# Kernel optimization log

Measured on AMD Instinct MI355X. Metric: run time of the kernel, lower is better.

The kernel has to match this reference:

```python
import jax, jax.numpy as jnp
import numpy as np

HEADS = 16
D_MODEL = 1024
IMG_MODEL = 512
D_K = D_MODEL // HEADS


def setup_inputs() -> dict:
    key = jax.random.key(0)
    ks = jax.random.split(key, 12)
    B, LQ, LKV = 8, 2048, 1024
    s_dm = 1.0 / np.sqrt(D_MODEL)
    s_im = 1.0 / np.sqrt(IMG_MODEL)
    return {
        "q": jax.random.normal(ks[0], (B, LQ, D_MODEL), jnp.float32),
        "k": jax.random.normal(ks[1], (B, LKV, IMG_MODEL), jnp.float32),
        "v": jax.random.normal(ks[2], (B, LKV, IMG_MODEL), jnp.float32),
        "Wq": jax.random.normal(ks[3], (D_MODEL, D_MODEL), jnp.float32) * s_dm,
        "bq": jnp.zeros((D_MODEL,), jnp.float32),
        "Wk": jax.random.normal(ks[4], (IMG_MODEL, D_MODEL), jnp.float32) * s_im,
        "bk": jnp.zeros((D_MODEL,), jnp.float32),
        "Wv": jax.random.normal(ks[5], (IMG_MODEL, D_MODEL), jnp.float32) * s_im,
        "bv": jnp.zeros((D_MODEL,), jnp.float32),
        "Wo": jax.random.normal(ks[6], (D_MODEL, D_MODEL), jnp.float32) * s_dm,
        "bo": jnp.zeros((D_MODEL,), jnp.float32),
    }


def reference(q, k, v, Wq, bq, Wk, bk, Wv, bv, Wo, bo):
    B, LQ, _ = q.shape
    LKV = k.shape[1]
    # projections -> [B, H, L, d_k]
    qh = (q @ Wq + bq).reshape(B, LQ, HEADS, D_K).transpose(0, 2, 1, 3)
    kh = (k @ Wk + bk).reshape(B, LKV, HEADS, D_K).transpose(0, 2, 1, 3)
    vh = (v @ Wv + bv).reshape(B, LKV, HEADS, D_K).transpose(0, 2, 1, 3)
    scale = 1.0 / np.sqrt(D_K)
    scores = jnp.einsum("bhqd,bhkd->bhqk", qh, kh) * scale  # [B,H,LQ,LKV]
    attn = jax.nn.softmax(scores, axis=-1)  # dropout = identity at eval
    out = jnp.einsum("bhqk,bhkd->bhqd", attn, vh)  # [B,H,LQ,d_k]
    concat = out.transpose(0, 2, 1, 3).reshape(B, LQ, D_MODEL)
    return concat @ Wo + bo
```

## Files before the change

### kernel.cpp

```cpp
#include <hip/hip_runtime.h>

typedef __bf16 bf16;
typedef __bf16 bf16x8 __attribute__((ext_vector_type(8)));
typedef __bf16 bf16x4 __attribute__((ext_vector_type(4)));
typedef float f32x4 __attribute__((ext_vector_type(4)));

constexpr int BB   = 8;
constexpr int LQ   = 2048;
constexpr int LKV  = 1024;
constexpr int DM   = 1024;
constexpr int DIMG = 512;
constexpr int H    = 16;
constexpr int DK   = 64;

__device__ inline void async16(const bf16* g, bf16* l) {
  __builtin_amdgcn_global_load_lds((const __attribute__((address_space(1))) void*)g,
                                   (__attribute__((address_space(3))) void*)l, 16, 0, 0);
}
__device__ inline float fexp2(float x) { return __builtin_amdgcn_exp2f(x); }

__global__ __launch_bounds__(256) void cvt_all(const float* __restrict__ q,
                                               const float* __restrict__ k,
                                               const float* __restrict__ v,
                                               bf16* __restrict__ qo,
                                               bf16* __restrict__ ko,
                                               bf16* __restrict__ vo,
                                               int nq4, int nk4) {
  int i = blockIdx.x * 256 + threadIdx.x;
  const float* in;
  bf16* out;
  int idx;
  if (i < nq4) { in = q; out = qo; idx = i; }
  else if (i < nq4 + nk4) { in = k; out = ko; idx = i - nq4; }
  else if (i < nq4 + 2 * nk4) { in = v; out = vo; idx = i - nq4 - nk4; }
  else return;
  const float4 f = ((const float4*)in)[idx];
  bf16x4 o;
  o[0] = (bf16)f.x; o[1] = (bf16)f.y; o[2] = (bf16)f.z; o[3] = (bf16)f.w;
  ((bf16x4*)out)[idx] = o;
}

__global__ __launch_bounds__(256) void transpose_all(const float* __restrict__ Wq,
                                                     const float* __restrict__ Wk,
                                                     const float* __restrict__ Wv,
                                                     const float* __restrict__ Wo,
                                                     bf16* __restrict__ WqT,
                                                     bf16* __restrict__ WkT,
                                                     bf16* __restrict__ WvT,
                                                     bf16* __restrict__ WoT) {
  const int z = blockIdx.z;
  const float* W;
  bf16* WT;
  int K;
  if (z == 0) { W = Wq; WT = WqT; K = DM; }
  else if (z == 1) { W = Wk; WT = WkT; K = DIMG; }
  else if (z == 2) { W = Wv; WT = WvT; K = DIMG; }
  else { W = Wo; WT = WoT; K = DM; }
  const int N = DM;
  if (blockIdx.x * 64 >= K) return;

  __shared__ float tile[64][65];
  const int k0 = blockIdx.x * 64, n0 = blockIdx.y * 64;
  const int tx = threadIdx.x & 63, tg = threadIdx.x >> 6;
#pragma unroll
  for (int i = 0; i < 16; ++i) {
    int row = tg * 16 + i;
    tile[row][tx] = W[(size_t)(k0 + row) * N + n0 + tx];
  }
  __syncthreads();
#pragma unroll
  for (int i = 0; i < 16; ++i) {
    int nrow = tg * 16 + i;
    WT[(size_t)(n0 + nrow) * K + k0 + tx] = (bf16)tile[tx][nrow];
  }
}

template <typename OutT, bool VT_OUT>
__device__ __forceinline__ void gemm_body(const bf16* __restrict__ A,
                                          const bf16* __restrict__ Bt,
                                          const float* __restrict__ bias,
                                          OutT* __restrict__ C,
                                          int N, int K, float oscale, int bm, int bn,
                                          bf16* As, bf16* Bs) {
  const int tid = threadIdx.x, lane = tid & 63, wave = tid >> 6;
  const int wm = (wave & 1) * 64, wn = (wave >> 1) * 64;
  const int fm = lane & 15, quad = lane >> 4, fk8 = quad * 8;

  f32x4 acc[4][4];
#pragma unroll
  for (int i = 0; i < 4; ++i)
#pragma unroll
    for (int j = 0; j < 4; ++j) {
      f32x4 z = {0.f, 0.f, 0.f, 0.f};
      acc[i][j] = z;
    }

  const int srow = lane >> 2, scol = (lane & 3) * 8;
  const bf16* ag0 = A + (size_t)(bm * 128 + wave * 16 + srow) * K + scol;
  const bf16* ag1 = ag0 + (size_t)64 * K;
  const bf16* bg0 = Bt + (size_t)(bn * 128 + wave * 16 + srow) * K + scol;
  const bf16* bg1 = bg0 + (size_t)64 * K;
  bf16* la0 = As + (wave * 16) * 32;
  bf16* la1 = As + (64 + wave * 16) * 32;
  bf16* lb0 = Bs + (wave * 16) * 32;
  bf16* lb1 = Bs + (64 + wave * 16) * 32;

  const int KT = K >> 5;
  async16(ag0, la0);
  async16(ag1, la1);
  async16(bg0, lb0);
  async16(bg1, lb1);
  __syncthreads();

  for (int t = 0; t < KT; ++t) {
    const int cur = (t & 1) * (128 * 32);
    if (t + 1 < KT) {
      const int nxt = ((t + 1) & 1) * (128 * 32);
      const int k0 = (t + 1) * 32;
      async16(ag0 + k0, la0 + nxt);
      async16(ag1 + k0, la1 + nxt);
      async16(bg0 + k0, lb0 + nxt);
      async16(bg1 + k0, lb1 + nxt);
    }
    bf16x8 af[4], bfr[4];
#pragma unroll
    for (int i = 0; i < 4; ++i)
      af[i] = *(const bf16x8*)&As[cur + (wm + i * 16 + fm) * 32 + fk8];
#pragma unroll
    for (int j = 0; j < 4; ++j)
      bfr[j] = *(const bf16x8*)&Bs[cur + (wn + j * 16 + fm) * 32 + fk8];
#pragma unroll
    for (int i = 0; i < 4; ++i)
#pragma unroll
      for (int j = 0; j < 4; ++j)
        acc[i][j] = __builtin_amdgcn_mfma_f32_16x16x32_bf16(af[i], bfr[j], acc[i][j], 0, 0, 0);
    __syncthreads();
  }

#pragma unroll
  for (int j = 0; j < 4; ++j) {
    const int col = bn * 128 + wn + j * 16 + fm;
    const float bv = bias[col];
    if constexpr (VT_OUT) {
      const int h = col >> 6, dk = col & 63;
#pragma unroll
      for (int i = 0; i < 4; ++i) {
        const int row = bm * 128 + wm + i * 16 + quad * 4;
        const int b = row >> 10, t = row & 1023;
        bf16x4 o;
#pragma unroll
        for (int r = 0; r < 4; ++r) o[r] = (bf16)((acc[i][j][r] + bv) * oscale);
        *(bf16x4*)&C[(((size_t)(b * H + h) * DK + dk) << 10) + t] = o;
      }
    } else {
#pragma unroll
      for (int i = 0; i < 4; ++i) {
#pragma unroll
        for (int r = 0; r < 4; ++r) {
          const int row = bm * 128 + wm + i * 16 + quad * 4 + r;
          C[(size_t)row * N + col] = (OutT)((acc[i][j][r] + bv) * oscale);
        }
      }
    }
  }
}

template <typename OutT>
__global__ __launch_bounds__(256) void gemm_one(const bf16* __restrict__ A,
                                                const bf16* __restrict__ Bt,
                                                const float* __restrict__ bias,
                                                OutT* __restrict__ C,
                                                int N, int K, float oscale) {
  __shared__ __align__(16) bf16 As[2 * 128 * 32];
  __shared__ __align__(16) bf16 Bs[2 * 128 * 32];
  const int cpx = gridDim.x >> 3;
  const int wg = ((int)blockIdx.x & 7) * cpx + ((int)blockIdx.x >> 3);
  const int nbn = N >> 7;
  gemm_body<OutT, false>(A, Bt, bias, C, N, K, oscale, wg / nbn, wg % nbn, As, Bs);
}

__global__ __launch_bounds__(256) void gemm_kv(const bf16* __restrict__ kbf,
                                               const bf16* __restrict__ WkT,
                                               const float* __restrict__ bk,
                                               bf16* __restrict__ kh,
                                               const bf16* __restrict__ vbf,
                                               const bf16* __restrict__ WvT,
                                               const float* __restrict__ bv,
                                               bf16* __restrict__ Vt) {
  __shared__ __align__(16) bf16 As[2 * 128 * 32];
  __shared__ __align__(16) bf16 Bs[2 * 128 * 32];
  const int cpx = gridDim.x >> 3;
  const int wg = ((int)blockIdx.x & 7) * cpx + ((int)blockIdx.x >> 3);
  const int bn = wg & 7;
  const int rest = wg >> 3;
  const int bm = rest & 63;
  if (rest < 64)
    gemm_body<bf16, false>(kbf, WkT, bk, kh, DM, DIMG, 1.0f, bm, bn, As, Bs);
  else
    gemm_body<bf16, true>(vbf, WvT, bv, Vt, DM, DIMG, 1.0f, bm, bn, As, Bs);
}

__global__ __launch_bounds__(512, 4) void attn_kernel(const bf16* __restrict__ qh,
                                                      const bf16* __restrict__ kh,
                                                      const bf16* __restrict__ vt,
                                                      bf16* __restrict__ out) {
  constexpr int NT = LKV / 64;
  __shared__ __align__(16) bf16 Ks[2][64 * 64];
  __shared__ __align__(16) bf16 Vs[2][64 * 64];
  __shared__ __align__(16) bf16 Ps[8][32 * 64];

  const int tid = threadIdx.x, lane = tid & 63, w = tid >> 6;
  const int fm = lane & 15, quad = lane >> 4;
  const int qt = blockIdx.x, h = blockIdx.y, b = blockIdx.z;
  const int q0 = qt * 256;

  const bf16* qbase = qh + ((size_t)(b * LQ) + q0 + w * 32) * DM + h * DK;
  const bf16* kbase = kh + (size_t)(b * LKV) * DM + h * DK;
  const bf16* vbase = vt + (size_t)(b * H + h) * DK * LKV;

  bf16x8 qf[2][2];
#pragma unroll
  for (int i = 0; i < 2; ++i)
#pragma unroll
    for (int kg = 0; kg < 2; ++kg)
      qf[i][kg] = *(const bf16x8*)&qbase[(size_t)(i * 16 + fm) * DM + kg * 32 + quad * 8];

  const int srow = lane >> 3, sslot = lane & 7;
  const int fs = fm & 7;

  auto stage = [&](int t, int bf) {
    const int r0 = w * 8;
    const int row = r0 + srow;
    const int gs = (sslot ^ (row & 7)) << 3;
    async16(kbase + (size_t)(t * 64 + row) * DM + gs, &Ks[bf][r0 * 64]);
    async16(vbase + (size_t)row * LKV + t * 64 + gs, &Vs[bf][r0 * 64]);
  };

  stage(0, 0);
  stage(1, 1);

  float row_m[2] = {-1e30f, -1e30f}, row_l[2] = {0.f, 0.f};
  f32x4 o_acc[2][4];
#pragma unroll
  for (int i = 0; i < 2; ++i)
#pragma unroll
    for (int jd = 0; jd < 4; ++jd) {
      f32x4 z = {0.f, 0.f, 0.f, 0.f};
      o_acc[i][jd] = z;
    }

  bf16* Pw = Ps[w];

#pragma unroll 2
  for (int t = 0; t < NT; ++t) {
    asm volatile("s_waitcnt vmcnt(2)" ::: "memory");
    __builtin_amdgcn_s_barrier();
    __builtin_amdgcn_sched_barrier(0);
    const bf16* Kb = Ks[t & 1];
    const bf16* Vb = Vs[t & 1];

    f32x4 s[4][2];
#pragma unroll
    for (int m = 0; m < 4; ++m)
#pragma unroll
      for (int i = 0; i < 2; ++i) {
        f32x4 z = {0.f, 0.f, 0.f, 0.f};
        s[m][i] = z;
      }
    __builtin_amdgcn_s_setprio(1);
#pragma unroll
    for (int kg = 0; kg < 2; ++kg)
#pragma unroll
      for (int m = 0; m < 4; ++m) {
        const bf16x8 kf =
            *(const bf16x8*)&Kb[(m * 16 + fm) * 64 + (((kg * 4 + quad) ^ fs) << 3)];
#pragma unroll
        for (int i = 0; i < 2; ++i)
          s[m][i] = __builtin_amdgcn_mfma_f32_16x16x32_bf16(kf, qf[i][kg], s[m][i], 0, 0, 0);
      }
    __builtin_amdgcn_s_setprio(0);

#pragma unroll
    for (int i = 0; i < 2; ++i) {
      float pm[4];
#pragma unroll
      for (int m = 0; m < 4; ++m)
        pm[m] = fmaxf(fmaxf(s[m][i][0], s[m][i][1]), fmaxf(s[m][i][2], s[m][i][3]));
      float mt = fmaxf(fmaxf(pm[0], pm[1]), fmaxf(pm[2], pm[3]));
      mt = fmaxf(mt, __shfl_xor(mt, 16));
      mt = fmaxf(mt, __shfl_xor(mt, 32));
      float alpha = 1.f;
      if (!__all(mt <= row_m[i] + 8.0f)) {
        const float nm = fmaxf(row_m[i], mt);
        alpha = fexp2(row_m[i] - nm);
        row_m[i] = nm;
#pragma unroll
        for (int r = 0; r < 4; ++r) {
          const float a_o = __shfl(alpha, quad * 4 + r);
#pragma unroll
          for (int jd = 0; jd < 4; ++jd) o_acc[i][jd][r] *= a_o;
        }
      }
      const float mi = row_m[i];
      float pp[4];
#pragma unroll
      for (int m = 0; m < 4; ++m) {
#pragma unroll
        for (int r = 0; r < 4; ++r) s[m][i][r] = fexp2(s[m][i][r] - mi);
        pp[m] = (s[m][i][0] + s[m][i][1]) + (s[m][i][2] + s[m][i][3]);
      }
      float ps = (pp[0] + pp[1]) + (pp[2] + pp[3]);
      ps += __shfl_xor(ps, 16);
      ps += __shfl_xor(ps, 32);
      row_l[i] = row_l[i] * alpha + ps;
    }

#pragma unroll
    for (int i = 0; i < 2; ++i)
#pragma unroll
      for (int m = 0; m < 4; ++m) {
        bf16x4 p4;
#pragma unroll
        for (int r = 0; r < 4; ++r) p4[r] = (bf16)s[m][i][r];
        *(bf16x4*)&Pw[(i * 16 + fm) * 64 + (((m * 2 + (quad >> 1)) ^ fs) << 3) +
                      ((quad & 1) << 2)] = p4;
      }

    __builtin_amdgcn_s_setprio(1);
#pragma unroll
    for (int kg = 0; kg < 2; ++kg) {
      bf16x8 pf[2];
#pragma unroll
      for (int i = 0; i < 2; ++i)
        pf[i] = *(const bf16x8*)&Pw[(i * 16 + fm) * 64 + (((kg * 4 + quad) ^ fs) << 3)];
#pragma unroll
      for (int jd = 0; jd < 4; ++jd) {
        const bf16x8 vfr =
            *(const bf16x8*)&Vb[(jd * 16 + fm) * 64 + (((kg * 4 + quad) ^ fs) << 3)];
#pragma unroll
        for (int i = 0; i < 2; ++i)
          o_acc[i][jd] = __builtin_amdgcn_mfma_f32_16x16x32_bf16(pf[i], vfr, o_acc[i][jd], 0, 0, 0);
      }
    }
    __builtin_amdgcn_s_setprio(0);

    __builtin_amdgcn_sched_barrier(0);
    __builtin_amdgcn_s_barrier();
    __builtin_amdgcn_sched_barrier(0);
    if (t < NT - 1) {
      const int tn = (t + 2 < NT) ? (t + 2) : (NT - 1);
      stage(tn, t & 1);
    }
  }
  asm volatile("s_waitcnt vmcnt(0)" ::: "memory");

  const float linv0 = 1.0f / row_l[0], linv1 = 1.0f / row_l[1];
  bf16* obase = out + ((size_t)(b * LQ) + q0 + w * 32) * DM + h * DK;
#pragma unroll
  for (int i = 0; i < 2; ++i) {
    const float li = i ? linv1 : linv0;
#pragma unroll
    for (int r = 0; r < 4; ++r) {
      const float lo = __shfl(li, quad * 4 + r);
#pragma unroll
      for (int jd = 0; jd < 4; ++jd)
        obase[(size_t)(i * 16 + quad * 4 + r) * DM + jd * 16 + fm] =
            (bf16)(o_acc[i][jd][r] * lo);
    }
  }
}

extern "C" void kernel_launch(void* const* d_in, const int* in_sizes, int n_in,
                              void* d_out, int out_size, void* d_ws, size_t ws_size,
                              hipStream_t stream) {
  const float* q  = (const float*)d_in[0];
  const float* k  = (const float*)d_in[1];
  const float* v  = (const float*)d_in[2];
  const float* Wq = (const float*)d_in[3];
  const float* bq = (const float*)d_in[4];
  const float* Wk = (const float*)d_in[5];
  const float* bk = (const float*)d_in[6];
  const float* Wv = (const float*)d_in[7];
  const float* bv = (const float*)d_in[8];
  const float* Wo = (const float*)d_in[9];
  const float* bo = (const float*)d_in[10];
  float* out = (float*)d_out;

  char* ws = (char*)d_ws;
  size_t off = 0;
  auto alloc = [&](size_t bytes) -> void* {
    void* p = ws + off;
    off += (bytes + 255) & ~(size_t)255;
    return p;
  };

  const size_t nq = (size_t)BB * LQ * DM;
  const size_t nk = (size_t)BB * LKV * DIMG;
  const size_t nkh = (size_t)BB * LKV * DM;

  bf16* qbf = (bf16*)alloc(nq * 2);
  bf16* kbf = (bf16*)alloc(nk * 2);
  bf16* vbf = (bf16*)alloc(nk * 2);
  bf16* WqT = (bf16*)alloc((size_t)DM * DM * 2);
  bf16* WkT = (bf16*)alloc((size_t)DM * DIMG * 2);
  bf16* WvT = (bf16*)alloc((size_t)DM * DIMG * 2);
  bf16* WoT = (bf16*)alloc((size_t)DM * DM * 2);
  bf16* qh  = (bf16*)alloc(nq * 2);
  bf16* kh  = (bf16*)alloc(nkh * 2);
  bf16* Vt  = (bf16*)alloc(nkh * 2);
  bf16* attn_out = qbf;

  const int nq4 = (int)(nq / 4), nk4 = (int)(nk / 4);
  cvt_all<<<(nq4 + 2 * nk4 + 255) / 256, 256, 0, stream>>>(q, k, v, qbf, kbf, vbf, nq4, nk4);

  transpose_all<<<dim3(DM / 64, DM / 64, 4), 256, 0, stream>>>(Wq, Wk, Wv, Wo, WqT, WkT, WvT, WoT);

  const float QSCALE = 0.125f * 1.44269504f;
  gemm_one<bf16><<<(BB * LQ / 128) * (DM / 128), 256, 0, stream>>>(
      qbf, WqT, bq, qh, DM, DM, QSCALE);
  gemm_kv<<<(BB * LKV / 128) * (DM / 128) * 2, 256, 0, stream>>>(
      kbf, WkT, bk, kh, vbf, WvT, bv, Vt);

  attn_kernel<<<dim3(LQ / 256, H, BB), 512, 0, stream>>>(qh, kh, Vt, attn_out);

  gemm_one<float><<<(BB * LQ / 128) * (DM / 128), 256, 0, stream>>>(
      attn_out, WoT, bo, out, BB * LQ == 0 ? DM : DM, DM, 1.0f);
}
```

Measured before the change: 399.4 us.

## Triple-buffer GEMM pipeline and merge prep and QKV projection launches

The GEMM main loop moves from a double-buffered LDS pipeline with two barriers per step to a three-slot ring. It issues loads two tiles ahead and uses a vmcnt wait plus one barrier per k-step, aiming to hide global-to-LDS latency. The conversion and weight-transpose kernels are merged into one launch, and the Q, K and V projection GEMMs are merged into one 2048-block launch, cutting launch gaps and tail effects. The extra LDS slot raises per-block shared memory, and the attention max reduction is reordered into a sequential chain.

```diff
diff --git a/kernel.cpp b/kernel.cpp
--- a/kernel.cpp
+++ b/kernel.cpp
@@ -19,36 +19,40 @@
 }
 __device__ inline float fexp2(float x) { return __builtin_amdgcn_exp2f(x); }
 
-__global__ __launch_bounds__(256) void cvt_all(const float* __restrict__ q,
-                                               const float* __restrict__ k,
-                                               const float* __restrict__ v,
-                                               bf16* __restrict__ qo,
-                                               bf16* __restrict__ ko,
-                                               bf16* __restrict__ vo,
-                                               int nq4, int nk4) {
-  int i = blockIdx.x * 256 + threadIdx.x;
-  const float* in;
-  bf16* out;
-  int idx;
-  if (i < nq4) { in = q; out = qo; idx = i; }
-  else if (i < nq4 + nk4) { in = k; out = ko; idx = i - nq4; }
-  else if (i < nq4 + 2 * nk4) { in = v; out = vo; idx = i - nq4 - nk4; }
-  else return;
-  const float4 f = ((const float4*)in)[idx];
-  bf16x4 o;
-  o[0] = (bf16)f.x; o[1] = (bf16)f.y; o[2] = (bf16)f.z; o[3] = (bf16)f.w;
-  ((bf16x4*)out)[idx] = o;
-}
-
-__global__ __launch_bounds__(256) void transpose_all(const float* __restrict__ Wq,
-                                                     const float* __restrict__ Wk,
-                                                     const float* __restrict__ Wv,
-                                                     const float* __restrict__ Wo,
-                                                     bf16* __restrict__ WqT,
-                                                     bf16* __restrict__ WkT,
-                                                     bf16* __restrict__ WvT,
-                                                     bf16* __restrict__ WoT) {
-  const int z = blockIdx.z;
+__global__ __launch_bounds__(256) void prep_all(const float* __restrict__ q,
+                                                const float* __restrict__ k,
+                                                const float* __restrict__ v,
+                                                bf16* __restrict__ qo,
+                                                bf16* __restrict__ ko,
+                                                bf16* __restrict__ vo,
+                                                int nq4, int nk4, int NC,
+                                                const float* __restrict__ Wq,
+                                                const float* __restrict__ Wk,
+                                                const float* __restrict__ Wv,
+                                                const float* __restrict__ Wo,
+                                                bf16* __restrict__ WqT,
+                                                bf16* __restrict__ WkT,
+                                                bf16* __restrict__ WvT,
+                                                bf16* __restrict__ WoT) {
+  __shared__ float tile[64][65];
+  const int bid = blockIdx.x;
+  if (bid < NC) {
+    int i = bid * 256 + threadIdx.x;
+    const float* in;
+    bf16* out;
+    int idx;
+    if (i < nq4) { in = q; out = qo; idx = i; }
+    else if (i < nq4 + nk4) { in = k; out = ko; idx = i - nq4; }
+    else if (i < nq4 + 2 * nk4) { in = v; out = vo; idx = i - nq4 - nk4; }
+    else return;
+    const float4 f = ((const float4*)in)[idx];
+    bf16x4 o;
+    o[0] = (bf16)f.x; o[1] = (bf16)f.y; o[2] = (bf16)f.z; o[3] = (bf16)f.w;
+    ((bf16x4*)out)[idx] = o;
+    return;
+  }
+  const int tbid = bid - NC;
+  const int bx = tbid & 15, by = (tbid >> 4) & 15, z = tbid >> 8;
   const float* W;
   bf16* WT;
   int K;
@@ -57,10 +61,9 @@
   else if (z == 2) { W = Wv; WT = WvT; K = DIMG; }
   else { W = Wo; WT = WoT; K = DM; }
   const int N = DM;
-  if (blockIdx.x * 64 >= K) return;
-
-  __shared__ float tile[64][65];
-  const int k0 = blockIdx.x * 64, n0 = blockIdx.y * 64;
+  if (bx * 64 >= K) return;
+
+  const int k0 = bx * 64, n0 = by * 64;
   const int tx = threadIdx.x & 63, tg = threadIdx.x >> 6;
 #pragma unroll
   for (int i = 0; i < 16; ++i) {
@@ -85,6 +88,7 @@
   const int tid = threadIdx.x, lane = tid & 63, wave = tid >> 6;
   const int wm = (wave & 1) * 64, wn = (wave >> 1) * 64;
   const int fm = lane & 15, quad = lane >> 4, fk8 = quad * 8;
+  constexpr int SLOT = 128 * 32;
 
   f32x4 acc[4][4];
 #pragma unroll
@@ -105,23 +109,28 @@
   bf16* lb0 = Bs + (wave * 16) * 32;
   bf16* lb1 = Bs + (64 + wave * 16) * 32;
 
+  auto stage = [&](int t, int slot) {
+    const int k0 = t * 32, so = slot * SLOT;
+    async16(ag0 + k0, la0 + so);
+    async16(ag1 + k0, la1 + so);
+    async16(bg0 + k0, lb0 + so);
+    async16(bg1 + k0, lb1 + so);
+  };
+
   const int KT = K >> 5;
-  async16(ag0, la0);
-  async16(ag1, la1);
-  async16(bg0, lb0);
-  async16(bg1, lb1);
-  __syncthreads();
+  stage(0, 0);
+  stage(1, 1);
 
   for (int t = 0; t < KT; ++t) {
-    const int cur = (t & 1) * (128 * 32);
-    if (t + 1 < KT) {
-      const int nxt = ((t + 1) & 1) * (128 * 32);
-      const int k0 = (t + 1) * 32;
-      async16(ag0 + k0, la0 + nxt);
-      async16(ag1 + k0, la1 + nxt);
-      async16(bg0 + k0, lb0 + nxt);
-      async16(bg1 + k0, lb1 + nxt);
-    }
+    asm volatile("s_waitcnt vmcnt(4)" ::: "memory");
+    __builtin_amdgcn_s_barrier();
+    __builtin_amdgcn_sched_barrier(0);
+    {
+      const int nt = t + 2;
+      if (nt < KT) stage(nt, nt % 3);
+      else if (nt == KT) stage(KT - 1, nt % 3);
+    }
+    const int cur = (t % 3) * SLOT;
     bf16x8 af[4], bfr[4];
 #pragma unroll
     for (int i = 0; i < 4; ++i)
@@ -134,8 +143,8 @@
 #pragma unroll
       for (int j = 0; j < 4; ++j)
         acc[i][j] = __builtin_amdgcn_mfma_f32_16x16x32_bf16(af[i], bfr[j], acc[i][j], 0, 0, 0);
-    __syncthreads();
-  }
+  }
+  asm volatile("s_waitcnt vmcnt(0)" ::: "memory");
 
 #pragma unroll
   for (int j = 0; j < 4; ++j) {
@@ -171,33 +180,40 @@
                                                 const float* __restrict__ bias,
                                                 OutT* __restrict__ C,
                                                 int N, int K, float oscale) {
-  __shared__ __align__(16) bf16 As[2 * 128 * 32];
-  __shared__ __align__(16) bf16 Bs[2 * 128 * 32];
+  __shared__ __align__(16) bf16 As[3 * 128 * 32];
+  __shared__ __align__(16) bf16 Bs[3 * 128 * 32];
   const int cpx = gridDim.x >> 3;
   const int wg = ((int)blockIdx.x & 7) * cpx + ((int)blockIdx.x >> 3);
   const int nbn = N >> 7;
   gemm_body<OutT, false>(A, Bt, bias, C, N, K, oscale, wg / nbn, wg % nbn, As, Bs);
 }
 
-__global__ __launch_bounds__(256) void gemm_kv(const bf16* __restrict__ kbf,
-                                               const bf16* __restrict__ WkT,
-                                               const float* __restrict__ bk,
-                                               bf16* __restrict__ kh,
-                                               const bf16* __restrict__ vbf,
-                                               const bf16* __restrict__ WvT,
-                                               const float* __restrict__ bv,
-                                               bf16* __restrict__ Vt) {
-  __shared__ __align__(16) bf16 As[2 * 128 * 32];
-  __shared__ __align__(16) bf16 Bs[2 * 128 * 32];
+__global__ __launch_bounds__(256) void gemm_qkv(const bf16* __restrict__ qbf,
+                                                const bf16* __restrict__ WqT,
+                                                const float* __restrict__ bq,
+                                                bf16* __restrict__ qh,
+                                                const bf16* __restrict__ kbf,
+                                                const bf16* __restrict__ WkT,
+                                                const float* __restrict__ bk,
+                                                bf16* __restrict__ kh,
+                                                const bf16* __restrict__ vbf,
+                                                const bf16* __restrict__ WvT,
+                                                const float* __restrict__ bv,
+                                                bf16* __restrict__ Vt,
+                                                float qscale) {
+  __shared__ __align__(16) bf16 As[3 * 128 * 32];
+  __shared__ __align__(16) bf16 Bs[3 * 128 * 32];
   const int cpx = gridDim.x >> 3;
   const int wg = ((int)blockIdx.x & 7) * cpx + ((int)blockIdx.x >> 3);
-  const int bn = wg & 7;
-  const int rest = wg >> 3;
-  const int bm = rest & 63;
-  if (rest < 64)
-    gemm_body<bf16, false>(kbf, WkT, bk, kh, DM, DIMG, 1.0f, bm, bn, As, Bs);
-  else
-    gemm_body<bf16, true>(vbf, WvT, bv, Vt, DM, DIMG, 1.0f, bm, bn, As, Bs);
+  if (wg < 1024) {
+    gemm_body<bf16, false>(qbf, WqT, bq, qh, DM, DM, qscale, wg >> 3, wg & 7, As, Bs);
+  } else if (wg < 1536) {
+    const int idx = wg - 1024;
+    gemm_body<bf16, false>(kbf, WkT, bk, kh, DM, DIMG, 1.0f, idx >> 3, idx & 7, As, Bs);
+  } else {
+    const int idx = wg - 1536;
+    gemm_body<bf16, true>(vbf, WvT, bv, Vt, DM, DIMG, 1.0f, idx >> 3, idx & 7, As, Bs);
+  }
 }
 
 __global__ __launch_bounds__(512, 4) void attn_kernel(const bf16* __restrict__ qh,
@@ -285,8 +301,8 @@
       float pm[4];
 #pragma unroll
       for (int m = 0; m < 4; ++m)
-        pm[m] = fmaxf(fmaxf(s[m][i][0], s[m][i][1]), fmaxf(s[m][i][2], s[m][i][3]));
-      float mt = fmaxf(fmaxf(pm[0], pm[1]), fmaxf(pm[2], pm[3]));
+        pm[m] = fmaxf(fmaxf(fmaxf(s[m][i][0], s[m][i][1]), s[m][i][2]), s[m][i][3]);
+      float mt = fmaxf(fmaxf(fmaxf(pm[0], pm[1]), pm[2]), pm[3]);
       mt = fmaxf(mt, __shfl_xor(mt, 16));
       mt = fmaxf(mt, __shfl_xor(mt, 32));
       float alpha = 1.f;
@@ -411,18 +427,17 @@
   bf16* attn_out = qbf;
 
   const int nq4 = (int)(nq / 4), nk4 = (int)(nk / 4);
-  cvt_all<<<(nq4 + 2 * nk4 + 255) / 256, 256, 0, stream>>>(q, k, v, qbf, kbf, vbf, nq4, nk4);
-
-  transpose_all<<<dim3(DM / 64, DM / 64, 4), 256, 0, stream>>>(Wq, Wk, Wv, Wo, WqT, WkT, WvT, WoT);
+  const int NC = (nq4 + 2 * nk4 + 255) / 256;
+  prep_all<<<NC + 1024, 256, 0, stream>>>(q, k, v, qbf, kbf, vbf, nq4, nk4, NC,
+                                          Wq, Wk, Wv, Wo, WqT, WkT, WvT, WoT);
 
   const float QSCALE = 0.125f * 1.44269504f;
-  gemm_one<bf16><<<(BB * LQ / 128) * (DM / 128), 256, 0, stream>>>(
-      qbf, WqT, bq, qh, DM, DM, QSCALE);
-  gemm_kv<<<(BB * LKV / 128) * (DM / 128) * 2, 256, 0, stream>>>(
-      kbf, WkT, bk, kh, vbf, WvT, bv, Vt);
+  gemm_qkv<<<2048, 256, 0, stream>>>(qbf, WqT, bq, qh,
+                                     kbf, WkT, bk, kh,
+                                     vbf, WvT, bv, Vt, QSCALE);
 
   attn_kernel<<<dim3(LQ / 256, H, BB), 512, 0, stream>>>(qh, kh, Vt, attn_out);
 
   gemm_one<float><<<(BB * LQ / 128) * (DM / 128), 256, 0, stream>>>(
-      attn_out, WoT, bo, out, BB * LQ == 0 ? DM : DM, DM, 1.0f);
-}
+      attn_out, WoT, bo, out, DM, DM, 1.0f);
+}
```

Measured after the change: 416.5 us. 1.04x slower.
